# Optimization experiments

Hardware: AMD Instinct MI355X
Metric: run time of the kernel (lower is better)

Reference implementation:

```python
import jax, jax.numpy as jnp
from jax import lax
import numpy as np

KS = 3
N = KS * KS
EPS = 1e-5


def conv2d(x, w, b=None, groups=1):
    out = lax.conv_general_dilated(x, w, (1, 1), 'SAME',
                                   feature_group_count=groups,
                                   dimension_numbers=('NCHW', 'OIHW', 'NCHW'))
    if b is not None:
        out = out + b[None, :, None, None]
    return out


def batchnorm(x, g, b):
    # training-mode BN (fresh nn.Module defaults to train): batch stats, biased var
    mu = x.mean((0, 2, 3), keepdims=True)
    var = ((x - mu) ** 2).mean((0, 2, 3), keepdims=True)
    return (x - mu) * lax.rsqrt(var + EPS) * g[None, :, None, None] + b[None, :, None, None]


def up2x_align_corners(x):
    # bilinear upsample, scale_factor=2, align_corners=True
    B, C, H, W = x.shape
    Ho, Wo = 2 * H, 2 * W

    def idx_w(n_in, n_out):
        c = jnp.arange(n_out, dtype=x.dtype) * ((n_in - 1) / (n_out - 1))
        i0 = jnp.clip(jnp.floor(c).astype(jnp.int32), 0, n_in - 2)
        t = c - i0.astype(x.dtype)
        return i0, t

    y0, ty = idx_w(H, Ho)
    x0, tx = idx_w(W, Wo)
    r = x[:, :, y0, :] * (1 - ty)[None, None, :, None] + x[:, :, y0 + 1, :] * ty[None, None, :, None]
    return r[:, :, :, x0] * (1 - tx) + r[:, :, :, x0 + 1] * tx


def gather_hw(xp, qx, qy):
    # xp: (B,C,Hp,Wp); qx,qy: (B,H,W,N) int -> (B,C,H,W,N)
    B, C, Hp, Wp = xp.shape
    flat = xp.reshape(B, C, Hp * Wp)
    idx = (qx * Wp + qy).reshape(B, 1, -1)
    idx = jnp.broadcast_to(idx, (B, C, idx.shape[-1]))
    return jnp.take_along_axis(flat, idx, axis=2).reshape(B, C, *qx.shape[1:])


def deform_conv(x, p_w, p_b, m_w, m_b, w):
    # modulated deformable conv v2 (4uiiurz1 impl), ks=3, stride=1, padding=1
    B, C, H, W = x.shape
    off = conv2d(x, p_w, p_b)                      # (B,2N,H,W)
    m = jax.nn.sigmoid(conv2d(x, m_w, m_b))        # (B,N,H,W)
    xp = jnp.pad(x, ((0, 0), (0, 0), (1, 1), (1, 1)))
    Hp, Wp = H + 2, W + 2
    off = jnp.transpose(off, (0, 2, 3, 1))         # (B,H,W,2N)
    pn_x = jnp.repeat(jnp.arange(-1, 2, dtype=x.dtype), KS)  # kernel row offsets, n=i*3+j
    pn_y = jnp.tile(jnp.arange(-1, 2, dtype=x.dtype), KS)
    p0_x = jnp.arange(1, H + 1, dtype=x.dtype)[None, :, None, None]
    p0_y = jnp.arange(1, W + 1, dtype=x.dtype)[None, None, :, None]
    px = p0_x + pn_x + off[..., :N]                # (B,H,W,N)
    py = p0_y + pn_y + off[..., N:]
    fx = jnp.floor(lax.stop_gradient(px))
    fy = jnp.floor(lax.stop_gradient(py))
    qx0 = jnp.clip(fx, 0, Hp - 1)
    qx1 = jnp.clip(fx + 1, 0, Hp - 1)
    qy0 = jnp.clip(fy, 0, Wp - 1)
    qy1 = jnp.clip(fy + 1, 0, Wp - 1)
    pxc = jnp.clip(px, 0, Hp - 1)
    pyc = jnp.clip(py, 0, Wp - 1)
    g_lt = (1 + (qx0 - pxc)) * (1 + (qy0 - pyc))
    g_rb = (1 - (qx1 - pxc)) * (1 - (qy1 - pyc))
    g_lb = (1 + (qx0 - pxc)) * (1 - (qy1 - pyc))
    g_rt = (1 - (qx1 - pxc)) * (1 + (qy0 - pyc))
    ix0, ix1 = qx0.astype(jnp.int32), qx1.astype(jnp.int32)
    iy0, iy1 = qy0.astype(jnp.int32), qy1.astype(jnp.int32)
    x_off = (g_lt[:, None] * gather_hw(xp, ix0, iy0)
             + g_rb[:, None] * gather_hw(xp, ix1, iy1)
             + g_lb[:, None] * gather_hw(xp, ix0, iy1)
             + g_rt[:, None] * gather_hw(xp, ix1, iy0))   # (B,C,H,W,N)
    x_off = x_off * jnp.transpose(m, (0, 2, 3, 1))[:, None]  # modulation
    O = w.shape[0]
    # equivalent to reshape to (B,C,H*ks,W*ks) then conv stride ks (bias=False)
    return jnp.einsum('bchwn,ocn->bohw', x_off, w.reshape(O, C, N))


def setup_inputs() -> dict:
    key = jax.random.key(0)
    ks = jax.random.split(key, 18)
    f = jnp.float32
    Cin, Cout = 256, 128
    inp = {
        'x1': jax.random.normal(ks[0], (8, 128, 32, 32), f),
        'x2': jax.random.normal(ks[1], (8, 128, 64, 64), f),
        'dsc_dw_w': jax.random.normal(ks[2], (Cin, 1, 3, 3), f) * 0.1,
        'dsc_dw_b': jax.random.normal(ks[3], (Cin,), f) * 0.05,
        'dsc_pw_w': jax.random.normal(ks[4], (Cout, Cin, 1, 1), f) * 0.05,
        'dsc_pw_b': jax.random.normal(ks[5], (Cout,), f) * 0.05,
        'p_w': jax.random.normal(ks[6], (2 * N, Cout, 3, 3), f) * 0.01,
        'p_b': jax.random.normal(ks[7], (2 * N,), f) * 0.01,
        'm_w': jax.random.normal(ks[8], (N, Cout, 3, 3), f) * 0.01,
        'm_b': jax.random.normal(ks[9], (N,), f) * 0.01,
        'dcn_w': jax.random.normal(ks[10], (Cout, Cout, 3, 3), f) * 0.05,
        'bn1_g': jnp.ones((Cout,), f),
        'bn1_b': jnp.zeros((Cout,), f),
        'dw2_w': jax.random.normal(ks[11], (Cout, 1, 3, 3), f) * 0.1,
        'dw2_b': jax.random.normal(ks[12], (Cout,), f) * 0.05,
        'bn2_g': jnp.ones((Cout,), f),
        'bn2_b': jnp.zeros((Cout,), f),
    }
    return inp


def reference(x1, x2, dsc_dw_w, dsc_dw_b, dsc_pw_w, dsc_pw_b, p_w, p_b, m_w, m_b,
              dcn_w, bn1_g, bn1_b, dw2_w, dw2_b, bn2_g, bn2_b):
    x1u = up2x_align_corners(x1)                 # (B,128,64,64); diffX=diffY=0 -> no pad
    x = jnp.concatenate([x2, x1u], axis=1)       # (B,256,64,64)
    h = conv2d(x, dsc_dw_w, dsc_dw_b, groups=x.shape[1])   # depthwise
    h = conv2d(h, dsc_pw_w, dsc_pw_b)                      # pointwise -> 128
    h = deform_conv(h, p_w, p_b, m_w, m_b, dcn_w)
    h = jax.nn.gelu(batchnorm(h, bn1_g, bn1_b), approximate=False)
    h = conv2d(h, dw2_w, dw2_b, groups=h.shape[1])         # depthwise k=3
    return jax.nn.relu(batchnorm(h, bn2_g, bn2_b))
```

## Files before the change

kernel.cpp:

```cpp
#include <hip/hip_runtime.h>
#include <math.h>

typedef const float* fp;
typedef __attribute__((ext_vector_type(8))) short short8;
typedef __attribute__((ext_vector_type(4))) float f32x4;

__device__ __forceinline__ unsigned short f2bf(float f){
    unsigned u = __float_as_uint(f);
    u += 0x7fff + ((u >> 16) & 1);
    return (unsigned short)(u >> 16);
}
__device__ __forceinline__ float bflo(unsigned u){ return __uint_as_float(u << 16); }
__device__ __forceinline__ float bfhi(unsigned u){ return __uint_as_float(u & 0xffff0000u); }

__global__ __launch_bounds__(256) void k_prep(fp dcn_w, fp pw, fp mw, fp pww,
                                              unsigned short* Wbf, unsigned short* Wpm,
                                              unsigned short* Wpwbf){
    int i = blockIdx.x*256 + threadIdx.x;
    if(i < 147456){
        int c = i & 127, o = (i >> 7) & 127, n = i >> 14;
        Wbf[i] = f2bf(dcn_w[o*1152 + c*9 + n]);
    } else if(i < 184320){
        int j = i - 147456;
        int c = j & 127, q = (j >> 7) & 31, n = j >> 12;
        float v = 0.f;
        if(q < 18)      v = pw[q*1152 + c*9 + n];
        else if(q < 27) v = mw[(q-18)*1152 + c*9 + n];
        Wpm[j] = f2bf(v);
    } else {
        int j = i - 184320;
        Wpwbf[j] = f2bf(pww[j]);
    }
}

__global__ __launch_bounds__(256) void k_updw256(fp x1, fp x2, fp w, fp bias, float* Bo){
    __shared__ float sA[66*68 + 4];
    int bid = blockIdx.x;
    int c = bid & 255, b = bid >> 8;
    int tid = threadIdx.x;
    for(int j = tid; j < 264; j += 256){
        int idx;
        if(j < 66)       idx = j;
        else if(j < 132) idx = 65*68 + (j-66);
        else if(j < 196) idx = (j-132+1)*68;
        else if(j < 260) idx = (j-196+1)*68 + 65;
        else             idx = 66*68 + (j-260);
        sA[idx] = 0.f;
    }
    if(c < 128){
        const float* src = x2 + ((size_t)(b*128+c)<<12);
        for(int j = tid; j < 1024; j += 256){
            int yy = j >> 4, x4 = (j & 15) << 2;
            float4 v = *(const float4*)&src[(yy<<6) + x4];
            float* d = &sA[(yy+1)*68 + x4 + 1];
            d[0]=v.x; d[1]=v.y; d[2]=v.z; d[3]=v.w;
        }
    } else {
        int cc = c - 128;
        fp src = x1 + ((b*128+cc)<<10);
        const float s = 31.0f/63.0f;
        for(int j = tid; j < 4096; j += 256){
            int yy = j >> 6, xx = j & 63;
            float fy = yy*s, fx = xx*s;
            int iy = (int)fy; if (iy > 30) iy = 30;
            int ix = (int)fx; if (ix > 30) ix = 30;
            float ty = fy - (float)iy, tx = fx - (float)ix;
            float v00 = src[iy*32+ix],     v01 = src[iy*32+ix+1];
            float v10 = src[(iy+1)*32+ix], v11 = src[(iy+1)*32+ix+1];
            sA[(yy+1)*68 + xx + 1] =
                (v00*(1.f-ty)+v10*ty)*(1.f-tx) + (v01*(1.f-ty)+v11*ty)*tx;
        }
    }
    __syncthreads();
    float w0=w[c*9+0], w1=w[c*9+1], w2=w[c*9+2];
    float w3=w[c*9+3], w4=w[c*9+4], w5=w[c*9+5];
    float w6=w[c*9+6], w7=w[c*9+7], w8=w[c*9+8];
    float bv = bias[c];
    float* dst = Bo + ((size_t)(b*256+c)<<12);
    for(int j = tid; j < 1024; j += 256){
        int y = j >> 4, x0 = (j & 15) << 2;
        float a0=bv, a1=bv, a2=bv, a3=bv;
        #pragma unroll
        for(int ky=0; ky<3; ky++){
            const float* rr = &sA[(y+ky)*68 + x0];
            float4 u0 = *(const float4*)&rr[0];
            float2 u1 = *(const float2*)&rr[4];
            float wA = (ky==0)?w0:((ky==1)?w3:w6);
            float wB = (ky==0)?w1:((ky==1)?w4:w7);
            float wC = (ky==0)?w2:((ky==1)?w5:w8);
            a0 += wA*u0.x + wB*u0.y + wC*u0.z;
            a1 += wA*u0.y + wB*u0.z + wC*u0.w;
            a2 += wA*u0.z + wB*u0.w + wC*u1.x;
            a3 += wA*u0.w + wB*u1.x + wC*u1.y;
        }
        *(float4*)&dst[(y<<6)+x0] = make_float4(a0,a1,a2,a3);
    }
}

#define PW_STAGE_X(kc, bufp) do{ \
    _Pragma("unroll") \
    for(int k_=0;k_<4;k_++){ \
        int j_ = tid + (k_<<9); \
        int cc_ = j_ >> 4, p4_ = (j_ & 15) << 2; \
        int c_ = ((kc)<<7) + cc_; \
        float4 v_ = *(const float4*)&Bo[((size_t)((b<<8)+c_)<<12) + pix0 + p4_]; \
        (bufp)[(p4_+0)*136 + cc_] = f2bf(v_.x); \
        (bufp)[(p4_+1)*136 + cc_] = f2bf(v_.y); \
        (bufp)[(p4_+2)*136 + cc_] = f2bf(v_.z); \
        (bufp)[(p4_+3)*136 + cc_] = f2bf(v_.w); \
    } }while(0)

#define PW_STAGE_W(kc) do{ \
    _Pragma("unroll") \
    for(int k_=0;k_<4;k_++){ \
        int j_ = tid + (k_<<9); \
        int o_ = j_ >> 4, cg_ = j_ & 15; \
        *(int4*)&sW[o_*136 + (cg_<<3)] = \
            *(const int4*)&Wpwbf[o_*256 + ((kc)<<7) + (cg_<<3)]; \
    } }while(0)

#define PW_DOMFMA(srcp) do{ \
    _Pragma("unroll") \
    for(int ks_=0; ks_<4; ks_++){ \
        int k0_ = ks_ << 5; \
        short8 bfr0 = *(const short8*)&(srcp)[(phb + m16)*136 + k0_ + (quad<<3)]; \
        short8 bfr1 = *(const short8*)&(srcp)[(phb + 16 + m16)*136 + k0_ + (quad<<3)]; \
        _Pragma("unroll") \
        for(int ot_=0;ot_<2;ot_++){ \
            short8 afr = *(const short8*)&sW[(wo + (ot_<<4) + m16)*136 + k0_ + (quad<<3)]; \
            acc[ot_][0] = __builtin_amdgcn_mfma_f32_16x16x32_bf16(afr, bfr0, acc[ot_][0], 0,0,0); \
            acc[ot_][1] = __builtin_amdgcn_mfma_f32_16x16x32_bf16(afr, bfr1, acc[ot_][1], 0,0,0); \
        } } }while(0)

__global__ __launch_bounds__(512, 4) void k_pw(const float* Bo, const unsigned short* Wpwbf,
                                               fp bias, unsigned short* Cbf){
    __shared__ __align__(16) unsigned short sW[128*136];
    __shared__ __align__(16) unsigned short sX[2][64*136];
    int b = blockIdx.x & 7;
    int pix0 = (blockIdx.x >> 3) << 6;
    int tid = threadIdx.x;
    int lane = tid & 63, wave = tid >> 6;
    int m16 = lane & 15, quad = lane >> 4;
    int wo  = (wave & 3) << 5;
    int phb = (wave >> 2) << 5;

    short8 ap = {0,0,0,0,0,0,0,0}, bpr = {0,0,0,0,0,0,0,0};
    if(quad == 0){
        ap[0]  = (short)f2bf((float)m16);
        bpr[0] = (short)f2bf((float)(m16+100));
    }
    f32x4 dp = {0.f,0.f,0.f,0.f};
    dp = __builtin_amdgcn_mfma_f32_16x16x32_bf16(ap, bpr, dp, 0,0,0);
    bool p1 = true;
    #pragma unroll
    for(int r=0;r<4;r++){
        float expP1 = (float)(quad*4+r) * (float)(m16+100);
        p1 = p1 && (fabsf(dp[r]-expP1) < 0.5f);
    }
    bool swapD = (__ballot(p1) != 0xFFFFFFFFFFFFFFFFull);

    f32x4 acc[2][2];
    #pragma unroll
    for(int i=0;i<2;i++){
        #pragma unroll
        for(int j=0;j<2;j++) acc[i][j] = (f32x4){0.f,0.f,0.f,0.f};
    }

    PW_STAGE_X(0, (&sX[0][0]));
    PW_STAGE_W(0);
    __syncthreads();
    PW_STAGE_X(1, (&sX[1][0]));
    PW_DOMFMA((&sX[0][0]));
    __syncthreads();
    PW_STAGE_W(1);
    __syncthreads();
    PW_DOMFMA((&sX[1][0]));

    if(!swapD){
        #pragma unroll
        for(int ot=0;ot<2;ot++){
            int o0 = wo + (ot<<4) + (quad<<2);
            float4 bv = *(const float4*)&bias[o0];
            #pragma unroll
            for(int pt=0;pt<2;pt++){
                int px = pix0 + phb + (pt<<4) + m16;
                unsigned long long pk = (unsigned long long)f2bf(acc[ot][pt][0] + bv.x)
                    | ((unsigned long long)f2bf(acc[ot][pt][1] + bv.y)<<16)
                    | ((unsigned long long)f2bf(acc[ot][pt][2] + bv.z)<<32)
                    | ((unsigned long long)f2bf(acc[ot][pt][3] + bv.w)<<48);
                *(unsigned long long*)&Cbf[((size_t)((b<<12) + px))*128 + o0] = pk;
            }
        }
    } else {
        #pragma unroll
        for(int ot=0;ot<2;ot++){
            int o = wo + (ot<<4) + m16;
            float bv = bias[o];
            #pragma unroll
            for(int pt=0;pt<2;pt++){
                #pragma unroll
                for(int r=0;r<4;r++){
                    int px = pix0 + phb + (pt<<4) + (quad<<2) + r;
                    Cbf[((size_t)((b<<12) + px))*128 + o] = f2bf(acc[ot][pt][r] + bv);
                }
            }
        }
    }
}

__global__ __launch_bounds__(256, 2) void k_offmask(const unsigned short* Cbf, const unsigned short* Wpm,
                                                    fp pb, fp mb, float* OM){
    __shared__ __align__(16) unsigned short sWin[3*66*136];
    __shared__ __align__(16) unsigned short sW[2][32*136];
    int b = blockIdx.x & 7;
    int y = blockIdx.x >> 3;
    int pix0 = y << 6;
    int tid = threadIdx.x;
    int lane = tid & 63, wave = tid >> 6;
    int m16 = lane & 15, quad = lane >> 4;
    int wp = wave << 4;
    const unsigned short* cbf = Cbf + ((size_t)b<<12)*128;

    short8 ap = {0,0,0,0,0,0,0,0}, bpr = {0,0,0,0,0,0,0,0};
    if(quad == 0){
        ap[0]  = (short)f2bf((float)m16);
        bpr[0] = (short)f2bf((float)(m16+100));
    }
    f32x4 dp = {0.f,0.f,0.f,0.f};
    dp = __builtin_amdgcn_mfma_f32_16x16x32_bf16(ap, bpr, dp, 0,0,0);
    bool p1 = true;
    #pragma unroll
    for(int r=0;r<4;r++){
        float expP1 = (float)(quad*4+r) * (float)(m16+100);
        p1 = p1 && (fabsf(dp[r]-expP1) < 0.5f);
    }
    bool swapD = (__ballot(p1) != 0xFFFFFFFFFFFFFFFFull);

    f32x4 acc[2];
    acc[0] = (f32x4){0.f,0.f,0.f,0.f};
    acc[1] = (f32x4){0.f,0.f,0.f,0.f};

    {
        const int4* wsrc = (const int4*)Wpm;
        int4 wA_ = wsrc[tid], wB_ = wsrc[tid + 256];
        for(int i = tid; i < 3168; i += 256){
            int pos = i >> 4, g = i & 15;
            int r = pos / 66, col = pos - r*66;
            int yy = y + r - 1, xx = col - 1;
            int4 v = make_int4(0,0,0,0);
            if(yy>=0 && yy<64 && xx>=0 && xx<64)
                v = *(const int4*)&cbf[(size_t)((yy<<6)+xx)*128 + (g<<3)];
            *(int4*)&sWin[pos*136 + (g<<3)] = v;
        }
        *(int4*)&sW[0][(tid>>4)*136 + ((tid&15)<<3)] = wA_;
        int j = tid + 256;
        *(int4*)&sW[0][(j>>4)*136 + ((j&15)<<3)] = wB_;
    }
    __syncthreads();

    for(int n=0;n<9;n++){
        int4 wA_, wB_;
        if(n<8){
            const int4* wsrc = (const int4*)(Wpm + ((n+1)<<12));
            wA_ = wsrc[tid]; wB_ = wsrc[tid + 256];
        }
        int ky = n/3, kx = n - ky*3;
        const unsigned short* base = &sWin[(ky*66 + wp + kx)*136];
        #pragma unroll
        for(int ks=0; ks<4; ks++){
            int k0 = ks << 5;
            short8 bfr = *(const short8*)&base[m16*136 + k0 + (quad<<3)];
            #pragma unroll
            for(int qt=0;qt<2;qt++){
                short8 afr = *(const short8*)&sW[n&1][((qt<<4) + m16)*136 + k0 + (quad<<3)];
                acc[qt] = __builtin_amdgcn_mfma_f32_16x16x32_bf16(afr, bfr, acc[qt], 0,0,0);
            }
        }
        if(n<8){
            *(int4*)&sW[(n+1)&1][(tid>>4)*136 + ((tid&15)<<3)] = wA_;
            int j = tid + 256;
            *(int4*)&sW[(n+1)&1][(j>>4)*136 + ((j&15)<<3)] = wB_;
        }
        __syncthreads();
    }
    if(!swapD){
        #pragma unroll
        for(int qt=0;qt<2;qt++){
            int px = pix0 + wp + m16;
            #pragma unroll
            for(int r=0;r<4;r++){
                int q = (qt<<4) + (quad<<2) + r;
                if(q < 27){
                    float v = acc[qt][r] + ((q<18) ? pb[q] : mb[q-18]);
                    if(q>=18) v = 1.f/(1.f+expf(-v));
                    OM[((b*27+q)<<12) + px] = v;
                }
            }
        }
    } else {
        #pragma unroll
        for(int qt=0;qt<2;qt++){
            int q = (qt<<4) + m16;
            if(q < 27){
                float bias = (q<18) ? pb[q] : mb[q-18];
                #pragma unroll
                for(int r=0;r<4;r++){
                    int px = pix0 + wp + (quad<<2) + r;
                    float v = acc[qt][r] + bias;
                    if(q>=18) v = 1.f/(1.f+expf(-v));
                    OM[((b*27+q)<<12) + px] = v;
                }
            }
        }
    }
}

#define K5_META(t) do{ if(tid < 256){ \
    int px_ = tid >> 2, k_ = tid & 3; \
    int pix_ = pix0 + px_; \
    int yq_ = pix_ >> 6, xq_ = pix_ & 63; \
    int kyy_ = (t)/3, kxx_ = (t)-kyy_*3; \
    float oxv_ = omb[((t)<<12)+pix_]; \
    float oyv_ = omb[(((t)+9)<<12)+pix_]; \
    float mv_  = omb[(((t)+18)<<12)+pix_]; \
    float pxf_ = (float)(yq_ + kyy_) + oxv_; \
    float pyf_ = (float)(xq_ + kxx_) + oyv_; \
    float fx_ = floorf(pxf_), fy_ = floorf(pyf_); \
    float qx0_ = fminf(fmaxf(fx_,0.f),65.f),  qx1_ = fminf(fmaxf(fx_+1.f,0.f),65.f); \
    float qy0_ = fminf(fmaxf(fy_,0.f),65.f),  qy1_ = fminf(fmaxf(fy_+1.f,0.f),65.f); \
    float pxc_ = fminf(fmaxf(pxf_,0.f),65.f), pyc_ = fminf(fmaxf(pyf_,0.f),65.f); \
    float dx0_ = 1.f+(qx0_-pxc_), dx1_ = 1.f-(qx1_-pxc_); \
    float dy0_ = 1.f+(qy0_-pyc_), dy1_ = 1.f-(qy1_-pyc_); \
    int ax0_=(int)qx0_, ax1_=(int)qx1_, ay0_=(int)qy0_, ay1_=(int)qy1_; \
    bool vx0_ = (ax0_>=1)&&(ax0_<=64), vx1_ = (ax1_>=1)&&(ax1_<=64); \
    bool vy0_ = (ay0_>=1)&&(ay0_<=64), vy1_ = (ay1_>=1)&&(ay1_<=64); \
    int  axs_ = (k_&1) ? ax1_ : ax0_; \
    int  ays_ = (k_==1||k_==2) ? ay1_ : ay0_; \
    bool vxs_ = (k_&1) ? vx1_ : vx0_; \
    bool vys_ = (k_==1||k_==2) ? vy1_ : vy0_; \
    float dxs_ = (k_&1) ? dx1_ : dx0_; \
    float dys_ = (k_==1||k_==2) ? dy1_ : dy0_; \
    bool v_ = vxs_ && vys_; \
    int base_ = v_ ? (((axs_-1)<<6)+(ays_-1)) : 0; \
    float g_ = v_ ? dxs_*dys_*mv_ : 0.f; \
    sM[tid] = make_uint2((unsigned)base_, __float_as_uint(g_)); \
} }while(0)

#define K5_GATHER(bufp) do{ \
    _Pragma("unroll") \
    for(int j_=0;j_<4;j_++){ \
        int px_ = pxb + (j_<<4); \
        uint2 e0_ = sM[(px_<<2)+0]; \
        uint2 e1_ = sM[(px_<<2)+1]; \
        uint2 e2_ = sM[(px_<<2)+2]; \
        uint2 e3_ = sM[(px_<<2)+3]; \
        float g0_ = __uint_as_float(e0_.y), g1_ = __uint_as_float(e1_.y); \
        float g2_ = __uint_as_float(e2_.y), g3_ = __uint_as_float(e3_.y); \
        uint2 c0_ = *(const uint2*)&cb[((size_t)e0_.x<<7) + cg4]; \
        uint2 c1_ = *(const uint2*)&cb[((size_t)e1_.x<<7) + cg4]; \
        uint2 c2_ = *(const uint2*)&cb[((size_t)e2_.x<<7) + cg4]; \
        uint2 c3_ = *(const uint2*)&cb[((size_t)e3_.x<<7) + cg4]; \
        float vx_ = g0_*bflo(c0_.x) + g1_*bflo(c1_.x) + g2_*bflo(c2_.x) + g3_*bflo(c3_.x); \
        float vy_ = g0_*bfhi(c0_.x) + g1_*bfhi(c1_.x) + g2_*bfhi(c2_.x) + g3_*bfhi(c3_.x); \
        float vz_ = g0_*bflo(c0_.y) + g1_*bflo(c1_.y) + g2_*bflo(c2_.y) + g3_*bflo(c3_.y); \
        float vw_ = g0_*bfhi(c0_.y) + g1_*bfhi(c1_.y) + g2_*bfhi(c2_.y) + g3_*bfhi(c3_.y); \
        unsigned long long pk_ = (unsigned long long)f2bf(vx_) \
            | ((unsigned long long)f2bf(vy_)<<16) \
            | ((unsigned long long)f2bf(vz_)<<32) \
            | ((unsigned long long)f2bf(vw_)<<48); \
        *(unsigned long long*)&(bufp)[px_*136 + cg4] = pk_; \
    } }while(0)

#define K5_STAGE_W(t) do{ \
    const int4* wsrc_ = (const int4*)(Wbf + ((t)<<14)); \
    _Pragma("unroll") \
    for(int k_=0;k_<4;k_++){ int j_ = tid + (k_<<9); \
        *(int4*)&sW[(j_>>4)*136 + ((j_&15)<<3)] = wsrc_[j_]; } }while(0)

#define K5_DOMFMA(srcp) do{ \
    _Pragma("unroll") \
    for(int ks_=0; ks_<4; ks_++){ \
        int k0_ = ks_ << 5; \
        short8 bfr0 = *(const short8*)&(srcp)[(phb + m16)*136 + k0_ + (quad<<3)]; \
        short8 bfr1 = *(const short8*)&(srcp)[(phb + 16 + m16)*136 + k0_ + (quad<<3)]; \
        _Pragma("unroll") \
        for(int ot_=0;ot_<2;ot_++){ \
            short8 afr = *(const short8*)&sW[(wo + (ot_<<4) + m16)*136 + k0_ + (quad<<3)]; \
            acc[ot_][0] = __builtin_amdgcn_mfma_f32_16x16x32_bf16(afr, bfr0, acc[ot_][0], 0,0,0); \
            acc[ot_][1] = __builtin_amdgcn_mfma_f32_16x16x32_bf16(afr, bfr1, acc[ot_][1], 0,0,0); \
        } } }while(0)

__global__ __launch_bounds__(512, 4) void k_deform(const unsigned short* Cbf, fp OM,
                                                   const unsigned short* Wbf,
                                                   float* D, float* stats){
    __shared__ __align__(16) unsigned short sW[128*136];
    __shared__ __align__(16) unsigned short sX[2][64*136];
    __shared__ __align__(8)  uint2 sM[256];
    int b = blockIdx.x & 7;
    int pix0 = (blockIdx.x >> 3) << 6;
    int tid = threadIdx.x;
    int lane = tid & 63, wave = tid >> 6;
    int m16 = lane & 15, quad = lane >> 4;
    int wo  = (wave & 3) << 5;
    int phb = (wave >> 2) << 5;
    int cg4 = (tid & 31) << 2;
    int pxb = tid >> 5;
    const float* omb = OM + b*27*4096;
    const unsigned short* cb = Cbf + ((size_t)b<<12)*128;

    short8 ap = {0,0,0,0,0,0,0,0}, bpr = {0,0,0,0,0,0,0,0};
    if(quad == 0){
        ap[0]  = (short)f2bf((float)m16);
        bpr[0] = (short)f2bf((float)(m16+100));
    }
    f32x4 dp = {0.f,0.f,0.f,0.f};
    dp = __builtin_amdgcn_mfma_f32_16x16x32_bf16(ap, bpr, dp, 0,0,0);
    bool p1 = true;
    #pragma unroll
    for(int r=0;r<4;r++){
        float expP1 = (float)(quad*4+r) * (float)(m16+100);
        p1 = p1 && (fabsf(dp[r]-expP1) < 0.5f);
    }
    bool swapD = (__ballot(p1) != 0xFFFFFFFFFFFFFFFFull);

    f32x4 acc[2][2];
    #pragma unroll
    for(int i=0;i<2;i++){
        #pragma unroll
        for(int j=0;j<2;j++) acc[i][j] = (f32x4){0.f,0.f,0.f,0.f};
    }

    K5_META(0);
    __syncthreads();
    K5_GATHER((&sX[0][0]));
    K5_STAGE_W(0);
    __syncthreads();
    K5_META(1);
    __syncthreads();

    for(int n=0;n<9;n++){
        if(n<8) K5_GATHER((&sX[(n+1)&1][0]));
        K5_DOMFMA((&sX[n&1][0]));
        __syncthreads();
        if(n<8){
            K5_STAGE_W(n+1);
            if(n<7) K5_META(n+2);
            __syncthreads();
        }
    }

    float* sdq = (float*)&sX[0][0];
    if(tid < 256) sdq[tid] = 0.f;
    __syncthreads();
    if(!swapD){
        #pragma unroll
        for(int ot=0;ot<2;ot++){
            #pragma unroll
            for(int pt=0;pt<2;pt++){
                int px = pix0 + phb + (pt<<4) + m16;
                #pragma unroll
                for(int r=0;r<4;r++){
                    int o = wo + (ot<<4) + (quad<<2) + r;
                    D[((b*128+o)<<12) + px] = acc[ot][pt][r];
                }
            }
        }
        #pragma unroll
        for(int ot=0;ot<2;ot++){
            #pragma unroll
            for(int r=0;r<4;r++){
                float s  = acc[ot][0][r] + acc[ot][1][r];
                float s2 = acc[ot][0][r]*acc[ot][0][r] + acc[ot][1][r]*acc[ot][1][r];
                #pragma unroll
                for(int msk=1; msk<16; msk<<=1){
                    s  += __shfl_xor(s, msk, 64);
                    s2 += __shfl_xor(s2, msk, 64);
                }
                if(m16 == 0){
                    int o = wo + (ot<<4) + (quad<<2) + r;
                    atomicAdd(&sdq[o], s);
                    atomicAdd(&sdq[128+o], s2);
                }
            }
        }
    } else {
        #pragma unroll
        for(int ot=0;ot<2;ot++){
            #pragma unroll
            for(int pt=0;pt<2;pt++){
                int o = wo + (ot<<4) + m16;
                #pragma unroll
                for(int r=0;r<4;r++){
                    int px = pix0 + phb + (pt<<4) + (quad<<2) + r;
                    D[((b*128+o)<<12) + px] = acc[ot][pt][r];
                }
            }
        }
        #pragma unroll
        for(int ot=0;ot<2;ot++){
            float s = 0.f, s2 = 0.f;
            #pragma unroll
            for(int pt=0;pt<2;pt++){
                #pragma unroll
                for(int r=0;r<4;r++){
                    float v = acc[ot][pt][r];
                    s += v; s2 += v*v;
                }
            }
            #pragma unroll
            for(int msk=16; msk<64; msk<<=1){
                s  += __shfl_xor(s, msk, 64);
                s2 += __shfl_xor(s2, msk, 64);
            }
            if(quad == 0){
                int o = wo + (ot<<4) + m16;
                atomicAdd(&sdq[o], s);
                atomicAdd(&sdq[128+o], s2);
            }
        }
    }
    __syncthreads();
    if(tid < 128){
        atomicAdd(&stats[tid],     sdq[tid]);
        atomicAdd(&stats[128+tid], sdq[128+tid]);
    }
}

__global__ __launch_bounds__(256) void k_bngelu_dw128(const float* Dsrc, float* stats,
                                                      fp g1, fp b1, fp w, fp bias, float* Hs){
    __shared__ float sG[66*68 + 4];
    __shared__ float sd[256], sq[256];
    int bid = blockIdx.x;
    int c = bid & 127, b = bid >> 7;
    int tid = threadIdx.x;
    float mean1 = stats[c] * (1.f/32768.f);
    float var1  = stats[128+c] * (1.f/32768.f) - mean1*mean1;
    float rstd1 = rsqrtf(var1 + 1e-5f);
    float sc = rstd1 * g1[c];
    float sb = b1[c] - mean1*sc;
    for(int j = tid; j < 264; j += 256){
        int idx;
        if(j < 66)       idx = j;
        else if(j < 132) idx = 65*68 + (j-66);
        else if(j < 196) idx = (j-132+1)*68;
        else if(j < 260) idx = (j-196+1)*68 + 65;
        else             idx = 66*68 + (j-260);
        sG[idx] = 0.f;
    }
    const float* dplane = Dsrc + ((size_t)(b*128+c)<<12);
    for(int j = tid; j < 1024; j += 256){
        int yy = j >> 4, x4 = (j & 15) << 2;
        float4 v = *(const float4*)&dplane[(yy<<6) + x4];
        float g0 = v.x*sc+sb, g1v = v.y*sc+sb, g2 = v.z*sc+sb, g3 = v.w*sc+sb;
        float* d = &sG[(yy+1)*68 + x4 + 1];
        d[0] = 0.5f*g0*(1.0f + erff(g0*0.70710678118654752f));
        d[1] = 0.5f*g1v*(1.0f + erff(g1v*0.70710678118654752f));
        d[2] = 0.5f*g2*(1.0f + erff(g2*0.70710678118654752f));
        d[3] = 0.5f*g3*(1.0f + erff(g3*0.70710678118654752f));
    }
    __syncthreads();
    float w0=w[c*9+0], w1=w[c*9+1], w2=w[c*9+2];
    float w3=w[c*9+3], w4=w[c*9+4], w5=w[c*9+5];
    float w6=w[c*9+6], w7=w[c*9+7], w8=w[c*9+8];
    float bv = bias[c];
    float* dst = Hs + ((size_t)(b*128+c)<<12);
    float s = 0.f, s2 = 0.f;
    for(int j = tid; j < 1024; j += 256){
        int y = j >> 4, x0 = (j & 15) << 2;
        float a0=bv, a1=bv, a2=bv, a3=bv;
        #pragma unroll
        for(int ky=0; ky<3; ky++){
            const float* rr = &sG[(y+ky)*68 + x0];
            float4 u0 = *(const float4*)&rr[0];
            float2 u1 = *(const float2*)&rr[4];
            float wA = (ky==0)?w0:((ky==1)?w3:w6);
            float wB = (ky==0)?w1:((ky==1)?w4:w7);
            float wC = (ky==0)?w2:((ky==1)?w5:w8);
            a0 += wA*u0.x + wB*u0.y + wC*u0.z;
            a1 += wA*u0.y + wB*u0.z + wC*u0.w;
            a2 += wA*u0.z + wB*u0.w + wC*u1.x;
            a3 += wA*u0.w + wB*u1.x + wC*u1.y;
        }
        *(float4*)&dst[(y<<6)+x0] = make_float4(a0,a1,a2,a3);
        s += a0+a1+a2+a3;
        s2 += a0*a0 + a1*a1 + a2*a2 + a3*a3;
    }
    sd[tid]=s; sq[tid]=s2; __syncthreads();
    for(int off=128; off>0; off>>=1){
        if(tid<off){ sd[tid]+=sd[tid+off]; sq[tid]+=sq[tid+off]; }
        __syncthreads();
    }
    if(tid==0){
        atomicAdd(&stats[256+c], sd[0]);
        atomicAdd(&stats[384+c], sq[0]);
    }
}

__global__ __launch_bounds__(256) void k_bn_relu_out(const float* Hs, const float* stats, fp g, fp bb, float* out){
    int idx = blockIdx.x*256+threadIdx.x;
    int c = (idx>>10)&127;
    float mean2 = stats[256+c] * (1.f/32768.f);
    float var2  = stats[384+c] * (1.f/32768.f) - mean2*mean2;
    float rs = rsqrtf(var2 + 1e-5f) * g[c];
    float sb = bb[c] - mean2*rs;
    float4 v = ((const float4*)Hs)[idx];
    float4 o;
    o.x = fmaxf(v.x*rs+sb, 0.f);
    o.y = fmaxf(v.y*rs+sb, 0.f);
    o.z = fmaxf(v.z*rs+sb, 0.f);
    o.w = fmaxf(v.w*rs+sb, 0.f);
    ((float4*)out)[idx] = o;
}

extern "C" void kernel_launch(void* const* d_in, const int* in_sizes, int n_in,
                              void* d_out, int out_size, void* d_ws, size_t ws_size,
                              hipStream_t stream){
    fp x1   = (fp)d_in[0];
    fp x2   = (fp)d_in[1];
    fp dw_w = (fp)d_in[2];  fp dw_b = (fp)d_in[3];
    fp pw_w = (fp)d_in[4];  fp pw_b = (fp)d_in[5];
    fp p_w  = (fp)d_in[6];  fp p_b  = (fp)d_in[7];
    fp m_w  = (fp)d_in[8];  fp m_b  = (fp)d_in[9];
    fp dcn_w= (fp)d_in[10];
    fp bn1g = (fp)d_in[11]; fp bn1b = (fp)d_in[12];
    fp dw2w = (fp)d_in[13]; fp dw2b = (fp)d_in[14];
    fp bn2g = (fp)d_in[15]; fp bn2b = (fp)d_in[16];

    float* ws  = (float*)d_ws;
    float* Bo  = ws;
    unsigned short* Cbf = (unsigned short*)(ws + 8388608);
    float* Hs  = ws + 8388608;
    float* OM  = ws + 12582912;
    unsigned short* Wbf = (unsigned short*)(ws + 13467648);
    unsigned short* Wpm = (unsigned short*)(ws + 13541376);
    float* stats = ws + 13559808;
    unsigned short* Wpwbf = (unsigned short*)(ws + 13560320);
    float* D   = Bo;
    float* out = (float*)d_out;

    hipMemsetAsync(stats, 0, 512*sizeof(float), stream);
    k_prep         <<<848,   256, 0, stream>>>(dcn_w, p_w, m_w, pw_w, Wbf, Wpm, Wpwbf);
    k_updw256      <<<2048,  256, 0, stream>>>(x1, x2, dw_w, dw_b, Bo);
    k_pw           <<<512,   512, 0, stream>>>(Bo, Wpwbf, pw_b, Cbf);
    k_offmask      <<<512,   256, 0, stream>>>(Cbf, Wpm, p_b, m_b, OM);
    k_deform       <<<512,   512, 0, stream>>>(Cbf, OM, Wbf, D, stats);
    k_bngelu_dw128 <<<1024,  256, 0, stream>>>(D, stats, bn1g, bn1b, dw2w, dw2b, Hs);
    k_bn_relu_out  <<<4096,  256, 0, stream>>>(Hs, stats, bn2g, bn2b, out);
}
```

Measured before the change: 205.5 us.

## Store intermediate activations in bf16 instead of fp32 across all stages

Result: faster. 200.4 us (-2.5%).

```diff
diff --git a/kernel.cpp b/kernel.cpp
--- a/kernel.cpp
+++ b/kernel.cpp
@@ -12,6 +12,10 @@
 }
 __device__ __forceinline__ float bflo(unsigned u){ return __uint_as_float(u << 16); }
 __device__ __forceinline__ float bfhi(unsigned u){ return __uint_as_float(u & 0xffff0000u); }
+__device__ __forceinline__ unsigned long long pk4(float a, float b, float c, float d){
+    return (unsigned long long)f2bf(a) | ((unsigned long long)f2bf(b)<<16)
+         | ((unsigned long long)f2bf(c)<<32) | ((unsigned long long)f2bf(d)<<48);
+}
 
 __global__ __launch_bounds__(256) void k_prep(fp dcn_w, fp pw, fp mw, fp pww,
                                               unsigned short* Wbf, unsigned short* Wpm,
@@ -33,7 +37,7 @@
     }
 }
 
-__global__ __launch_bounds__(256) void k_updw256(fp x1, fp x2, fp w, fp bias, float* Bo){
+__global__ __launch_bounds__(256) void k_updw256(fp x1, fp x2, fp w, fp bias, unsigned short* Bo){
     __shared__ float sA[66*68 + 4];
     int bid = blockIdx.x;
     int c = bid & 255, b = bid >> 8;
@@ -76,7 +80,7 @@
     float w3=w[c*9+3], w4=w[c*9+4], w5=w[c*9+5];
     float w6=w[c*9+6], w7=w[c*9+7], w8=w[c*9+8];
     float bv = bias[c];
-    float* dst = Bo + ((size_t)(b*256+c)<<12);
+    unsigned short* dst = Bo + ((size_t)(b*256+c)<<12);
     for(int j = tid; j < 1024; j += 256){
         int y = j >> 4, x0 = (j & 15) << 2;
         float a0=bv, a1=bv, a2=bv, a3=bv;
@@ -93,7 +97,7 @@
             a2 += wA*u0.z + wB*u0.w + wC*u1.x;
             a3 += wA*u0.w + wB*u1.x + wC*u1.y;
         }
-        *(float4*)&dst[(y<<6)+x0] = make_float4(a0,a1,a2,a3);
+        *(unsigned long long*)&dst[(y<<6)+x0] = pk4(a0,a1,a2,a3);
     }
 }
 
@@ -103,11 +107,11 @@
         int j_ = tid + (k_<<9); \
         int cc_ = j_ >> 4, p4_ = (j_ & 15) << 2; \
         int c_ = ((kc)<<7) + cc_; \
-        float4 v_ = *(const float4*)&Bo[((size_t)((b<<8)+c_)<<12) + pix0 + p4_]; \
-        (bufp)[(p4_+0)*136 + cc_] = f2bf(v_.x); \
-        (bufp)[(p4_+1)*136 + cc_] = f2bf(v_.y); \
-        (bufp)[(p4_+2)*136 + cc_] = f2bf(v_.z); \
-        (bufp)[(p4_+3)*136 + cc_] = f2bf(v_.w); \
+        uint2 v_ = *(const uint2*)&Bo[((size_t)((b<<8)+c_)<<12) + pix0 + p4_]; \
+        (bufp)[(p4_+0)*136 + cc_] = (unsigned short)(v_.x & 0xffffu); \
+        (bufp)[(p4_+1)*136 + cc_] = (unsigned short)(v_.x >> 16); \
+        (bufp)[(p4_+2)*136 + cc_] = (unsigned short)(v_.y & 0xffffu); \
+        (bufp)[(p4_+3)*136 + cc_] = (unsigned short)(v_.y >> 16); \
     } }while(0)
 
 #define PW_STAGE_W(kc) do{ \
@@ -132,7 +136,7 @@
             acc[ot_][1] = __builtin_amdgcn_mfma_f32_16x16x32_bf16(afr, bfr1, acc[ot_][1], 0,0,0); \
         } } }while(0)
 
-__global__ __launch_bounds__(512, 4) void k_pw(const float* Bo, const unsigned short* Wpwbf,
+__global__ __launch_bounds__(512, 4) void k_pw(const unsigned short* Bo, const unsigned short* Wpwbf,
                                                fp bias, unsigned short* Cbf){
     __shared__ __align__(16) unsigned short sW[128*136];
     __shared__ __align__(16) unsigned short sX[2][64*136];
@@ -184,11 +188,9 @@
             #pragma unroll
             for(int pt=0;pt<2;pt++){
                 int px = pix0 + phb + (pt<<4) + m16;
-                unsigned long long pk = (unsigned long long)f2bf(acc[ot][pt][0] + bv.x)
-                    | ((unsigned long long)f2bf(acc[ot][pt][1] + bv.y)<<16)
-                    | ((unsigned long long)f2bf(acc[ot][pt][2] + bv.z)<<32)
-                    | ((unsigned long long)f2bf(acc[ot][pt][3] + bv.w)<<48);
-                *(unsigned long long*)&Cbf[((size_t)((b<<12) + px))*128 + o0] = pk;
+                *(unsigned long long*)&Cbf[((size_t)((b<<12) + px))*128 + o0] =
+                    pk4(acc[ot][pt][0]+bv.x, acc[ot][pt][1]+bv.y,
+                        acc[ot][pt][2]+bv.z, acc[ot][pt][3]+bv.w);
             }
         }
     } else {
@@ -364,11 +366,7 @@
         float vy_ = g0_*bfhi(c0_.x) + g1_*bfhi(c1_.x) + g2_*bfhi(c2_.x) + g3_*bfhi(c3_.x); \
         float vz_ = g0_*bflo(c0_.y) + g1_*bflo(c1_.y) + g2_*bflo(c2_.y) + g3_*bflo(c3_.y); \
         float vw_ = g0_*bfhi(c0_.y) + g1_*bfhi(c1_.y) + g2_*bfhi(c2_.y) + g3_*bfhi(c3_.y); \
-        unsigned long long pk_ = (unsigned long long)f2bf(vx_) \
-            | ((unsigned long long)f2bf(vy_)<<16) \
-            | ((unsigned long long)f2bf(vz_)<<32) \
-            | ((unsigned long long)f2bf(vw_)<<48); \
-        *(unsigned long long*)&(bufp)[px_*136 + cg4] = pk_; \
+        *(unsigned long long*)&(bufp)[px_*136 + cg4] = pk4(vx_,vy_,vz_,vw_); \
     } }while(0)
 
 #define K5_STAGE_W(t) do{ \
@@ -392,7 +390,7 @@
 
 __global__ __launch_bounds__(512, 4) void k_deform(const unsigned short* Cbf, fp OM,
                                                    const unsigned short* Wbf,
-                                                   float* D, float* stats){
+                                                   unsigned short* D, float* stats){
     __shared__ __align__(16) unsigned short sW[128*136];
     __shared__ __align__(16) unsigned short sX[2][64*136];
     __shared__ __align__(8)  uint2 sM[256];
@@ -461,7 +459,7 @@
                 #pragma unroll
                 for(int r=0;r<4;r++){
                     int o = wo + (ot<<4) + (quad<<2) + r;
-                    D[((b*128+o)<<12) + px] = acc[ot][pt][r];
+                    D[((size_t)(b*128+o)<<12) + px] = f2bf(acc[ot][pt][r]);
                 }
             }
         }
@@ -492,7 +490,7 @@
                 #pragma unroll
                 for(int r=0;r<4;r++){
                     int px = pix0 + phb + (pt<<4) + (quad<<2) + r;
-                    D[((b*128+o)<<12) + px] = acc[ot][pt][r];
+                    D[((size_t)(b*128+o)<<12) + px] = f2bf(acc[ot][pt][r]);
                 }
             }
         }
@@ -526,8 +524,8 @@
     }
 }
 
-__global__ __launch_bounds__(256) void k_bngelu_dw128(const float* Dsrc, float* stats,
-                                                      fp g1, fp b1, fp w, fp bias, float* Hs){
+__global__ __launch_bounds__(256) void k_bngelu_dw128(const unsigned short* Dsrc, float* stats,
+                                                      fp g1, fp b1, fp w, fp bias, unsigned short* Hs){
     __shared__ float sG[66*68 + 4];
     __shared__ float sd[256], sq[256];
     int bid = blockIdx.x;
@@ -547,11 +545,12 @@
         else             idx = 66*68 + (j-260);
         sG[idx] = 0.f;
     }
-    const float* dplane = Dsrc + ((size_t)(b*128+c)<<12);
+    const unsigned short* dplane = Dsrc + ((size_t)(b*128+c)<<12);
     for(int j = tid; j < 1024; j += 256){
         int yy = j >> 4, x4 = (j & 15) << 2;
-        float4 v = *(const float4*)&dplane[(yy<<6) + x4];
-        float g0 = v.x*sc+sb, g1v = v.y*sc+sb, g2 = v.z*sc+sb, g3 = v.w*sc+sb;
+        uint2 v = *(const uint2*)&dplane[(yy<<6) + x4];
+        float g0 = bflo(v.x)*sc+sb, g1v = bfhi(v.x)*sc+sb;
+        float g2 = bflo(v.y)*sc+sb, g3 = bfhi(v.y)*sc+sb;
         float* d = &sG[(yy+1)*68 + x4 + 1];
         d[0] = 0.5f*g0*(1.0f + erff(g0*0.70710678118654752f));
         d[1] = 0.5f*g1v*(1.0f + erff(g1v*0.70710678118654752f));
@@ -563,7 +562,7 @@
     float w3=w[c*9+3], w4=w[c*9+4], w5=w[c*9+5];
     float w6=w[c*9+6], w7=w[c*9+7], w8=w[c*9+8];
     float bv = bias[c];
-    float* dst = Hs + ((size_t)(b*128+c)<<12);
+    unsigned short* dst = Hs + ((size_t)(b*128+c)<<12);
     float s = 0.f, s2 = 0.f;
     for(int j = tid; j < 1024; j += 256){
         int y = j >> 4, x0 = (j & 15) << 2;
@@ -581,7 +580,7 @@
             a2 += wA*u0.z + wB*u0.w + wC*u1.x;
             a3 += wA*u0.w + wB*u1.x + wC*u1.y;
         }
-        *(float4*)&dst[(y<<6)+x0] = make_float4(a0,a1,a2,a3);
+        *(unsigned long long*)&dst[(y<<6)+x0] = pk4(a0,a1,a2,a3);
         s += a0+a1+a2+a3;
         s2 += a0*a0 + a1*a1 + a2*a2 + a3*a3;
     }
@@ -596,19 +595,20 @@
     }
 }
 
-__global__ __launch_bounds__(256) void k_bn_relu_out(const float* Hs, const float* stats, fp g, fp bb, float* out){
+__global__ __launch_bounds__(256) void k_bn_relu_out(const unsigned short* Hs, const float* stats,
+                                                     fp g, fp bb, float* out){
     int idx = blockIdx.x*256+threadIdx.x;
     int c = (idx>>10)&127;
     float mean2 = stats[256+c] * (1.f/32768.f);
     float var2  = stats[384+c] * (1.f/32768.f) - mean2*mean2;
     float rs = rsqrtf(var2 + 1e-5f) * g[c];
     float sb = bb[c] - mean2*rs;
-    float4 v = ((const float4*)Hs)[idx];
+    uint2 v = ((const uint2*)Hs)[idx];
     float4 o;
-    o.x = fmaxf(v.x*rs+sb, 0.f);
-    o.y = fmaxf(v.y*rs+sb, 0.f);
-    o.z = fmaxf(v.z*rs+sb, 0.f);
-    o.w = fmaxf(v.w*rs+sb, 0.f);
+    o.x = fmaxf(bflo(v.x)*rs+sb, 0.f);
+    o.y = fmaxf(bfhi(v.x)*rs+sb, 0.f);
+    o.z = fmaxf(bflo(v.y)*rs+sb, 0.f);
+    o.w = fmaxf(bfhi(v.y)*rs+sb, 0.f);
     ((float4*)out)[idx] = o;
 }
 
@@ -627,15 +627,15 @@
     fp bn2g = (fp)d_in[15]; fp bn2b = (fp)d_in[16];
 
     float* ws  = (float*)d_ws;
-    float* Bo  = ws;
+    unsigned short* Bo  = (unsigned short*)ws;
     unsigned short* Cbf = (unsigned short*)(ws + 8388608);
-    float* Hs  = ws + 8388608;
+    unsigned short* Hs  = (unsigned short*)(ws + 8388608);
     float* OM  = ws + 12582912;
     unsigned short* Wbf = (unsigned short*)(ws + 13467648);
     unsigned short* Wpm = (unsigned short*)(ws + 13541376);
     float* stats = ws + 13559808;
     unsigned short* Wpwbf = (unsigned short*)(ws + 13560320);
-    float* D   = Bo;
+    unsigned short* D   = Bo;
     float* out = (float*)d_out;
 
     hipMemsetAsync(stats, 0, 512*sizeof(float), stream);
```
